# Performance work log

Hardware: AMD Instinct MI355X
Metric: run time of the kernel (lower is better)

Reference implementation:

```python
import jax, jax.numpy as jnp
import numpy as np

N_STATE = 256   # complex state size n (real state is 2n)
N_IN = 128
BATCH = 16
T_STEPS = 2048
H_STEP = 0.01
EPS = 1e-3
LAM_RE_MIN, LAM_RE_MAX, MAX_PHASE = -5.0, -0.5, 6.283


def setup_inputs() -> dict:
    rng = np.random.default_rng(0)
    n, nu = N_STATE, N_IN
    # trainable params (as in torch __init__)
    u1 = rng.random(n)
    u2 = rng.random(n) * 2.0 - 1.0
    alpha = np.log(-(u1 * (LAM_RE_MAX - LAM_RE_MIN) + LAM_RE_MIN)).astype(np.float32)
    theta = (MAX_PHASE * u2).astype(np.float32)
    B_re = (rng.standard_normal((n, nu)) / np.sqrt(2.0 * nu)).astype(np.float32)
    B_im = (rng.standard_normal((n, nu)) / np.sqrt(2.0 * nu)).astype(np.float32)
    # fixed basis-change buffers: rho (normalized), T_inv, P = rho @ T_inv, Pinv
    H1 = rng.standard_normal((n, n))
    H2 = rng.standard_normal((n, n))
    rho = np.block([[H1, -H2], [H2, H1]])
    rho = rho / np.linalg.norm(rho)
    I = np.eye(n)
    T_inv = (1.0 / np.sqrt(2.0)) * np.block([[I, I], [-1j * I, 1j * I]])
    P = rho.astype(np.complex128) @ T_inv
    Pinv = np.linalg.inv(P)
    key = jax.random.key(0)
    k1, k2 = jax.random.split(key)
    return {
        "xi_init": jax.random.normal(k1, (BATCH, 1, 2 * n), dtype=jnp.float32),
        "u_log": jax.random.normal(k2, (BATCH, T_STEPS, nu), dtype=jnp.float32),
        "alpha": jnp.asarray(alpha),
        "theta": jnp.asarray(theta),
        "B_re": jnp.asarray(B_re),
        "B_im": jnp.asarray(B_im),
        "P_re": jnp.asarray(P.real, dtype=jnp.float32),
        "P_im": jnp.asarray(P.imag, dtype=jnp.float32),
        "Pinv_re": jnp.asarray(Pinv.real, dtype=jnp.float32),
        "Pinv_im": jnp.asarray(Pinv.imag, dtype=jnp.float32),
        "T": T_STEPS,
    }


def reference(xi_init, u_log, alpha, theta, B_re, B_im, P_re, P_im, Pinv_re, Pinv_im, T):
    n = alpha.shape[0]
    lam = (-jnp.exp(alpha) - EPS) + 1j * theta          # (n,) complex64
    Bc = B_re + 1j * B_im                               # (n, nu)
    P = P_re + 1j * P_im                                # (2n, 2n)
    Pinv = Pinv_re + 1j * Pinv_im                       # (2n, 2n)
    xi0 = xi_init[:, 0, :]                              # (B, 2n) real

    def step(xi, u_t):
        # xi: (B, 2n) real state; u_t: (B, nu)
        x_tilde = xi.astype(jnp.complex64) @ Pinv.T     # (B, 2n) complex
        x_bar = x_tilde[:, :n]                          # (B, n)
        x_bar_dot = lam * x_bar + u_t.astype(jnp.complex64) @ Bc.T
        x_tilde_dot = jnp.concatenate([x_bar_dot, jnp.conj(x_bar_dot)], axis=-1)
        x_dot = (x_tilde_dot @ P.T).real                # (B, 2n)
        xi_new = xi + H_STEP * x_dot
        return xi_new, xi_new

    u_seq = jnp.swapaxes(u_log, 0, 1)                   # (T, B, nu)
    _, xs = jax.lax.scan(step, xi0, u_seq)              # (T, B, 2n)
    # torch _sim logs xi_init, then skips xi after t=0, logs xi after t=1..T-1
    x_log = jnp.concatenate([xi0[None], xs[1:]], axis=0)  # (T, B, 2n)
    return jnp.swapaxes(x_log, 0, 1)                    # (B, T, 2n)
```

## Files before the change

### kernel.cpp

```cpp
#include <hip/hip_runtime.h>
#include <hip/hip_bf16.h>
#include <cstddef>
#include <cstdint>

#define N_ST 256
#define TWO_N 512
#define NU 128
#define BATCH 16
#define TSTEPS 2048
#define MTOT (BATCH * TSTEPS)
#define H_STEP 0.01f
#define EPS_V 0.001f
#define NCHUNK 32
#define CHUNKL 64

typedef __attribute__((ext_vector_type(4))) float f32x4;
typedef __attribute__((ext_vector_type(4))) short s16x4;
typedef __attribute__((ext_vector_type(8))) short s16x8;

#define AS1 __attribute__((address_space(1)))
#define AS3 __attribute__((address_space(3)))

#define OFF_FPK    0
#define OFF_ZPK    8388608
#define OFF_UPK    16777216
#define OFF_WT     18874368
#define OFF_WF     19005440
#define OFF_D      19038208
#define OFF_XBAR0  19039232
#define OFF_E      19047424

static __device__ __forceinline__ float bf2f(short s) {
    return __uint_as_float(((unsigned)(unsigned short)s) << 16);
}
static __device__ __forceinline__ short f2bf(float f) {
    __hip_bfloat16 b = __float2bfloat16(f);
    return *reinterpret_cast<short*>(&b);
}

__global__ __launch_bounds__(256) void prep_mega(
    const float* __restrict__ P_re, const float* __restrict__ P_im,
    const float* __restrict__ B_re, const float* __restrict__ B_im,
    const float* __restrict__ alpha, const float* __restrict__ theta,
    const float* __restrict__ Pinv_re, const float* __restrict__ Pinv_im,
    const float* __restrict__ xi0, const float* __restrict__ u,
    short* __restrict__ Wtpk, short* __restrict__ Wfpk,
    float* __restrict__ dbuf, float* __restrict__ xbar0,
    short* __restrict__ upk)
{
    __shared__ float xs[BATCH * TWO_N];
    int blk = blockIdx.x, tid = threadIdx.x;
    if (blk < 1024) {
        int idx = blk * 256 + tid;
        int j = idx >> 9, c = idx & 511;
        float v;
        if (c < N_ST) v = P_re[j * TWO_N + c] + P_re[j * TWO_N + c + N_ST];
        else          v = P_im[j * TWO_N + c] - P_im[j * TWO_N + c - N_ST];
        Wtpk[((size_t)(j >> 4) * TWO_N + c) * 16 + (j & 15)] = f2bf(v);
    } else if (blk < 1280) {
        int idx = (blk - 1024) * 256 + tid;
        int k = idx >> 9, c = idx & 511;
        float v = (c < N_ST) ? B_re[c * NU + k] : B_im[(c - N_ST) * NU + k];
        Wfpk[((size_t)(c >> 4) * NU + k) * 16 + (c & 15)] = f2bf(H_STEP * v);
    } else if (blk == 1280) {
        int i = tid;
        float dr = 1.0f + H_STEP * (-expf(alpha[i]) - EPS_V);
        float di = H_STEP * theta[i];
        float pr = 1.0f, pi = 0.0f;
        for (int k = 0; k < CHUNKL; ++k) { float nr = pr * dr - pi * di; pi = pr * di + pi * dr; pr = nr; }
        dbuf[i] = dr; dbuf[N_ST + i] = di; dbuf[2 * N_ST + i] = pr; dbuf[3 * N_ST + i] = pi;
    } else if (blk < 1345) {
#pragma unroll
        for (int q = 0; q < 8; ++q)
            *reinterpret_cast<float4*>(&xs[(q * 256 + tid) * 4]) =
                *reinterpret_cast<const float4*>(&xi0[(q * 256 + tid) * 4]);
        __syncthreads();
        int wv = tid >> 6, l = tid & 63;
        int i = (blk - 1281) * 4 + wv;
        float rp[BATCH] = {}, ip[BATCH] = {};
#pragma unroll
        for (int q = 0; q < 8; ++q) {
            int j = q * 64 + l;
            float pr = Pinv_re[(size_t)i * TWO_N + j];
            float pi = Pinv_im[(size_t)i * TWO_N + j];
#pragma unroll
            for (int b = 0; b < BATCH; ++b) {
                float x = xs[b * TWO_N + j];
                rp[b] = fmaf(pr, x, rp[b]);
                ip[b] = fmaf(pi, x, ip[b]);
            }
        }
#pragma unroll
        for (int m = 1; m < 64; m <<= 1) {
#pragma unroll
            for (int b = 0; b < BATCH; ++b) {
                rp[b] += __shfl_xor(rp[b], m, 64);
                ip[b] += __shfl_xor(ip[b], m, 64);
            }
        }
        if (l == 0) {
#pragma unroll
            for (int b = 0; b < BATCH; ++b) {
                xbar0[b * TWO_N + i] = rp[b];
                xbar0[b * TWO_N + N_ST + i] = ip[b];
            }
        }
    } else {
        short* st = (short*)xs;
        int bid = blk - 1345;
        const float* up = u + (size_t)bid * 8192;
#pragma unroll
        for (int q = 0; q < 8; ++q) {
            int idx = q * 1024 + tid * 4;
            float4 v = *reinterpret_cast<const float4*>(up + idx);
            int m = idx >> 7, k = idx & 127;
            s16x4 pv;
            pv[0] = f2bf(v.x); pv[1] = f2bf(v.y); pv[2] = f2bf(v.z); pv[3] = f2bf(v.w);
            *reinterpret_cast<__shared__ s16x4*>(&st[m * 132 + k]) = pv;
        }
        __syncthreads();
        short* op = upk + (size_t)bid * 8192;
#pragma unroll
        for (int q2 = 0; q2 < 4; ++q2) {
            int o = q2 * 2048 + tid * 8;
            int ml = o & 15, k = (o >> 4) & 127, sl = o >> 11;
            s16x8 w;
#pragma unroll
            for (int r = 0; r < 8; ++r) w[r] = st[(sl * 16 + ml + r) * 132 + k];
            *reinterpret_cast<s16x8*>(op + o) = w;
        }
    }
}

__global__ __launch_bounds__(512, 2) void chunk_fgemm(
    const short* __restrict__ upk, const short* __restrict__ Wfpk,
    const float* __restrict__ dbuf, short* __restrict__ Fpk,
    float* __restrict__ e)
{
    __shared__ __align__(1024) short lds[36864];
    char* smem = (char*)lds;
    const int tid = threadIdx.x;
    const int w = tid >> 6, lane = tid & 63;
    const int laneL = lane & 15, laneH = lane >> 4;
    const int cid = blockIdx.x;
    const unsigned ldsA = (unsigned)(uintptr_t)(AS3 short*)&lds[0];
    f32x4 acc[4][4] = {};

#define STG(buf, kk)                                                                                \
    do {                                                                                            \
        _Pragma("unroll")                                                                           \
        for (int q_ = 0; q_ < 4; ++q_) {                                                            \
            int sb_ = w + q_ * 8;                                                                   \
            __builtin_amdgcn_global_load_lds(                                                       \
                (const AS1 void*)(Wfpk + (size_t)sb_ * 2048 + (size_t)(kk) * 16 + lane * 8),        \
                (AS3 void*)(smem + 8192 + (buf) * 32768 + sb_ * 1024), 16, 0, 0);                   \
        }                                                                                           \
        if (w < 4) {                                                                                \
            __builtin_amdgcn_global_load_lds(                                                       \
                (const AS1 void*)(upk + (size_t)(cid * 4 + w) * 2048 + (size_t)(kk) * 16 + lane * 8), \
                (AS3 void*)(smem + (buf) * 4096 + w * 1024), 16, 0, 0);                             \
        }                                                                                           \
    } while (0)

    STG(0, 0);
#pragma unroll
    for (int t = 0; t < 4; ++t) {
        const int buf = t & 1;
        if (t < 3) STG(buf ^ 1, (t + 1) * 32);
        if (t < 3) {
            if (w < 4) asm volatile("s_waitcnt vmcnt(5)" ::: "memory");
            else       asm volatile("s_waitcnt vmcnt(4)" ::: "memory");
        } else {
            asm volatile("s_waitcnt vmcnt(0)" ::: "memory");
        }
        __builtin_amdgcn_sched_barrier(0);
        __builtin_amdgcn_s_barrier();
        __builtin_amdgcn_sched_barrier(0);

        s16x4 al[4], ah[4], bl[4], bh[4];
#pragma unroll
        for (int i = 0; i < 4; ++i) {
            unsigned ad = ldsA + (unsigned)buf * 4096u + (unsigned)i * 1024u + ((unsigned)lane << 3);
            asm volatile("ds_read_b64_tr_b16 %0, %1 offset:0"   : "=v"(al[i]) : "v"(ad));
            asm volatile("ds_read_b64_tr_b16 %0, %1 offset:512" : "=v"(ah[i]) : "v"(ad));
        }
#pragma unroll
        for (int j = 0; j < 4; ++j) {
            unsigned bd = ldsA + 8192u + (unsigned)buf * 32768u + ((unsigned)(w * 4 + j) << 10) + ((unsigned)lane << 3);
            asm volatile("ds_read_b64_tr_b16 %0, %1 offset:0"   : "=v"(bl[j]) : "v"(bd));
            asm volatile("ds_read_b64_tr_b16 %0, %1 offset:512" : "=v"(bh[j]) : "v"(bd));
        }
        asm volatile("s_waitcnt lgkmcnt(0)" ::: "memory");
        __builtin_amdgcn_sched_barrier(0);
        __builtin_amdgcn_s_barrier();
        __builtin_amdgcn_sched_barrier(0);

        __builtin_amdgcn_s_setprio(1);
#pragma unroll
        for (int i = 0; i < 4; ++i) {
            s16x8 av = __builtin_shufflevector(al[i], ah[i], 0, 1, 2, 3, 4, 5, 6, 7);
#pragma unroll
            for (int j = 0; j < 4; ++j) {
                s16x8 bv = __builtin_shufflevector(bl[j], bh[j], 0, 1, 2, 3, 4, 5, 6, 7);
                acc[i][j] = __builtin_amdgcn_mfma_f32_16x16x32_bf16(av, bv, acc[i][j], 0, 0, 0);
            }
        }
        __builtin_amdgcn_s_setprio(0);
    }
#undef STG

    const int g4 = laneH * 4;
#pragma unroll
    for (int i = 0; i < 4; ++i) {
        size_t slab = (size_t)(cid * 4 + i);
#pragma unroll
        for (int j = 0; j < 4; ++j) {
            int n = w * 64 + j * 16 + laneL;
            s16x4 pv;
#pragma unroll
            for (int r = 0; r < 4; ++r) pv[r] = f2bf(acc[i][j][r]);
            *reinterpret_cast<s16x4*>(Fpk + slab * 8192 + (size_t)n * 16 + g4) = pv;
        }
    }
#pragma unroll
    for (int i = 0; i < 4; ++i) {
#pragma unroll
        for (int j = 0; j < 4; ++j) {
            int s = w * 64 + j * 16 + laneL;
#pragma unroll
            for (int r = 0; r < 4; ++r) {
                int t = i * 16 + laneH * 4 + r;
                *(short*)(smem + t * 1024 + (((unsigned)(2 * s)) ^ (unsigned)((t & 15) << 3))) =
                    f2bf(acc[i][j][r]);
            }
        }
    }
    __syncthreads();
    if (tid < 256) {
        const int i2 = tid;
        float dr = dbuf[i2], di = dbuf[N_ST + i2];
        float re = 0.f, im = 0.f;
        const unsigned colr = (unsigned)(2 * i2);
#pragma unroll 8
        for (int t = 0; t < CHUNKL; ++t) {
            char* p = smem + t * 1024 + (colr ^ (unsigned)((t & 15) << 3));
            float fr = bf2f(*(short*)p);
            float fi = bf2f(*(short*)(p + 512));
            float nre = fmaf(dr, re, fmaf(-di, im, fr));
            float nim = fmaf(dr, im, fmaf(di, re, fi));
            re = nre; im = nim;
        }
        e[(size_t)cid * TWO_N + i2] = re;
        e[(size_t)cid * TWO_N + N_ST + i2] = im;
    }
}

__global__ __launch_bounds__(256) void scan_passC(const short* __restrict__ Fpk,
                                                  const float* __restrict__ dbuf,
                                                  const float* __restrict__ e,
                                                  const float* __restrict__ xbar0,
                                                  short* __restrict__ Zpk) {
    int b = blockIdx.x, c = blockIdx.y, i = threadIdx.x;
    float dr = dbuf[i], di = dbuf[N_ST + i];
    float dLr = dbuf[2 * N_ST + i], dLi = dbuf[3 * N_ST + i];
    float re = xbar0[b * TWO_N + i], im = xbar0[b * TWO_N + N_ST + i];
    for (int cc = 0; cc < c; ++cc) {
        size_t o = ((size_t)(b * NCHUNK + cc)) * TWO_N;
        float er = e[o + i], ei = e[o + N_ST + i];
        float nre = fmaf(dLr, re, fmaf(-dLi, im, er));
        float nim = fmaf(dLr, im, fmaf(dLi, re, ei));
        re = nre; im = nim;
    }
    int slab0 = (b * TSTEPS + c * CHUNKL) >> 4;
#pragma unroll
    for (int g = 0; g < 4; ++g) {
        const short* base = Fpk + (size_t)(slab0 + g) * 8192 + i * 16;
        s16x8 r0 = *reinterpret_cast<const s16x8*>(base);
        s16x8 r1 = *reinterpret_cast<const s16x8*>(base + 8);
        s16x8 i0 = *reinterpret_cast<const s16x8*>(base + 4096);
        s16x8 i1 = *reinterpret_cast<const s16x8*>(base + 4096 + 8);
        s16x8 zr0, zr1, zi0, zi1;
#pragma unroll
        for (int j = 0; j < 16; ++j) {
            float fr = bf2f(j < 8 ? r0[j & 7] : r1[j & 7]);
            float fi = bf2f(j < 8 ? i0[j & 7] : i1[j & 7]);
            float nre = fmaf(dr, re, fmaf(-di, im, fr));
            float nim = fmaf(dr, im, fmaf(di, re, fi));
            re = nre; im = nim;
            if (j < 8) { zr0[j & 7] = f2bf(re); zi0[j & 7] = f2bf(im); }
            else       { zr1[j & 7] = f2bf(re); zi1[j & 7] = f2bf(im); }
        }
        short* zb = Zpk + (size_t)(slab0 + g) * 8192 + i * 16;
        *reinterpret_cast<s16x8*>(zb)            = zr0;
        *reinterpret_cast<s16x8*>(zb + 8)        = zr1;
        *reinterpret_cast<s16x8*>(zb + 4096)     = zi0;
        *reinterpret_cast<s16x8*>(zb + 4096 + 8) = zi1;
    }
}

__global__ __launch_bounds__(512, 2) void gemm_out(const short* __restrict__ Apk,
                                                   const short* __restrict__ Bpk,
                                                   float* __restrict__ Cf,
                                                   const float* __restrict__ xi0) {
    __shared__ __align__(1024) short lds[49152];
    const int tid = threadIdx.x;
    const int wid = tid >> 6, lane = tid & 63;
    const int l = blockIdx.x;
    const int mb = ((l >> 4) << 3) | (l & 7);
    const int nb = (l >> 3) & 1;
    const int m0 = mb * 256, n0 = nb * 256;
    const int wm = wid >> 2, wn = wid & 3;
    f32x4 acc[8][4] = {};
    const size_t slabStride = (size_t)TWO_N * 16;
    const unsigned ldsBase = (unsigned)(uintptr_t)(AS3 short*)&lds[0];
    constexpr int NT = TWO_N / 32;

#define STAGE(buf, kk)                                                                              \
    do {                                                                                            \
        const short* gA0 = Apk + ((size_t)(m0 >> 4) + wid)     * slabStride + (size_t)(kk) * 16 + lane * 8; \
        const short* gA1 = Apk + ((size_t)(m0 >> 4) + wid + 8) * slabStride + (size_t)(kk) * 16 + lane * 8; \
        const short* gB0 = Bpk + ((size_t)(n0 >> 4) + wid)     * slabStride + (size_t)(kk) * 16 + lane * 8; \
        const short* gB1 = Bpk + ((size_t)(n0 >> 4) + wid + 8) * slabStride + (size_t)(kk) * 16 + lane * 8; \
        __builtin_amdgcn_global_load_lds((const AS1 void*)gA0,                                      \
            (AS3 void*)&lds[(buf) * 8192 + wid * 512], 16, 0, 0);                                   \
        __builtin_amdgcn_global_load_lds((const AS1 void*)gA1,                                      \
            (AS3 void*)&lds[(buf) * 8192 + (wid + 8) * 512], 16, 0, 0);                             \
        __builtin_amdgcn_global_load_lds((const AS1 void*)gB0,                                      \
            (AS3 void*)&lds[24576 + (buf) * 8192 + wid * 512], 16, 0, 0);                           \
        __builtin_amdgcn_global_load_lds((const AS1 void*)gB1,                                      \
            (AS3 void*)&lds[24576 + (buf) * 8192 + (wid + 8) * 512], 16, 0, 0);                     \
    } while (0)

    STAGE(0, 0);
    STAGE(1, 32);

#pragma unroll
    for (int t = 0; t < NT; ++t) {
        const int cur = t % 3;
        if (t + 2 < NT) STAGE((t + 2) % 3, (t + 2) * 32);

        if (t + 2 < NT)      asm volatile("s_waitcnt vmcnt(8)" ::: "memory");
        else if (t + 1 < NT) asm volatile("s_waitcnt vmcnt(4)" ::: "memory");
        else                 asm volatile("s_waitcnt vmcnt(0)" ::: "memory");
        __builtin_amdgcn_sched_barrier(0);
        __builtin_amdgcn_s_barrier();
        __builtin_amdgcn_sched_barrier(0);

        s16x4 al[8], ah[8], bl[4], bh[4];
        const unsigned aB = ldsBase + (unsigned)cur * 16384u;
        const unsigned bB = ldsBase + 49152u + (unsigned)cur * 16384u;
#pragma unroll
        for (int i = 0; i < 8; ++i) {
            unsigned ad = aB + ((unsigned)(wm * 8 + i) << 10) + ((unsigned)lane << 3);
            asm volatile("ds_read_b64_tr_b16 %0, %1 offset:0"   : "=v"(al[i]) : "v"(ad));
            asm volatile("ds_read_b64_tr_b16 %0, %1 offset:512" : "=v"(ah[i]) : "v"(ad));
        }
#pragma unroll
        for (int j = 0; j < 4; ++j) {
            unsigned bd = bB + ((unsigned)(wn * 4 + j) << 10) + ((unsigned)lane << 3);
            asm volatile("ds_read_b64_tr_b16 %0, %1 offset:0"   : "=v"(bl[j]) : "v"(bd));
            asm volatile("ds_read_b64_tr_b16 %0, %1 offset:512" : "=v"(bh[j]) : "v"(bd));
        }
        asm volatile("s_waitcnt lgkmcnt(0)" ::: "memory");
        __builtin_amdgcn_sched_barrier(0);
        __builtin_amdgcn_s_barrier();
        __builtin_amdgcn_sched_barrier(0);

        __builtin_amdgcn_s_setprio(1);
#pragma unroll
        for (int i = 0; i < 8; ++i) {
            s16x8 av = __builtin_shufflevector(al[i], ah[i], 0, 1, 2, 3, 4, 5, 6, 7);
#pragma unroll
            for (int j = 0; j < 4; ++j) {
                s16x8 bv = __builtin_shufflevector(bl[j], bh[j], 0, 1, 2, 3, 4, 5, 6, 7);
                acc[i][j] = __builtin_amdgcn_mfma_f32_16x16x32_bf16(av, bv, acc[i][j], 0, 0, 0);
            }
        }
        __builtin_amdgcn_s_setprio(0);
    }
#undef STAGE

    const int cn = lane & 15;
    const int g4 = (lane >> 4) * 4;
#pragma unroll
    for (int i = 0; i < 8; ++i) {
        int mrow = m0 + wm * 128 + i * 16 + g4;
#pragma unroll
        for (int j = 0; j < 4; ++j) {
            int ncol = n0 + wn * 64 + j * 16 + cn;
            float* cp = Cf + (size_t)mrow * TWO_N + ncol;
#pragma unroll
            for (int r = 0; r < 4; ++r) {
                float v = acc[i][j][r];
                if (((mrow + r) & (TSTEPS - 1)) == 0)
                    v = xi0[((mrow + r) >> 11) * TWO_N + ncol];
                cp[(size_t)r * TWO_N] = v;
            }
        }
    }
}

extern "C" void kernel_launch(void* const* d_in, const int* in_sizes, int n_in,
                              void* d_out, int out_size, void* d_ws, size_t ws_size,
                              hipStream_t stream) {
    const float* xi_init = (const float*)d_in[0];
    const float* u_log   = (const float*)d_in[1];
    const float* alpha   = (const float*)d_in[2];
    const float* theta   = (const float*)d_in[3];
    const float* B_re    = (const float*)d_in[4];
    const float* B_im    = (const float*)d_in[5];
    const float* P_re    = (const float*)d_in[6];
    const float* P_im    = (const float*)d_in[7];
    const float* Pinv_re = (const float*)d_in[8];
    const float* Pinv_im = (const float*)d_in[9];
    float* out = (float*)d_out;
    float* ws  = (float*)d_ws;

    short* Fpk  = (short*)(ws + OFF_FPK);
    short* Zpk  = (short*)(ws + OFF_ZPK);
    short* upk  = (short*)(ws + OFF_UPK);
    short* Wtpk = (short*)(ws + OFF_WT);
    short* Wfpk = (short*)(ws + OFF_WF);
    float* dbuf  = ws + OFF_D;
    float* xbar0 = ws + OFF_XBAR0;
    float* e     = ws + OFF_E;

    prep_mega<<<1857, 256, 0, stream>>>(P_re, P_im, B_re, B_im, alpha, theta,
                                        Pinv_re, Pinv_im, xi_init, u_log,
                                        Wtpk, Wfpk, dbuf, xbar0, upk);

    chunk_fgemm<<<MTOT / CHUNKL, 512, 0, stream>>>(upk, Wfpk, dbuf, Fpk, e);

    scan_passC<<<dim3(BATCH, NCHUNK), 256, 0, stream>>>(Fpk, dbuf, e, xbar0, Zpk);

    gemm_out<<<256, 512, 0, stream>>>(Zpk, Wtpk, out, xi_init);
}
```

Baseline: 71.78 us.

## Recompute chunk GEMM in second pass and fuse scan, dropping F buffer

Replaces the separate F-buffer write and scan_passC kernel with a templated chunk kernel launched twice. The first pass computes chunk end-states e. The second recomputes the chunk GEMM, carries the prefix across chunks, and scans directly from LDS to emit Z. This removes the round trip of the large bf16 F intermediate through global memory. In exchange the input GEMM and the u loads are done twice.

```diff
diff --git a/kernel.cpp b/kernel.cpp
--- a/kernel.cpp
+++ b/kernel.cpp
@@ -21,14 +21,13 @@
 #define AS1 __attribute__((address_space(1)))
 #define AS3 __attribute__((address_space(3)))
 
-#define OFF_FPK    0
-#define OFF_ZPK    8388608
-#define OFF_UPK    16777216
-#define OFF_WT     18874368
-#define OFF_WF     19005440
-#define OFF_D      19038208
-#define OFF_XBAR0  19039232
-#define OFF_E      19047424
+#define OFF_ZPK    0
+#define OFF_UPK    8388608
+#define OFF_WT     10485760
+#define OFF_WF     10616832
+#define OFF_D      10649600
+#define OFF_XBAR0  10650624
+#define OFF_E      10658816
 
 static __device__ __forceinline__ float bf2f(short s) {
     return __uint_as_float(((unsigned)(unsigned short)s) << 16);
@@ -132,10 +131,11 @@
     }
 }
 
-__global__ __launch_bounds__(512, 2) void chunk_fgemm(
+template <bool EMITZ>
+__global__ __launch_bounds__(512, 2) void chunk_fs(
     const short* __restrict__ upk, const short* __restrict__ Wfpk,
-    const float* __restrict__ dbuf, short* __restrict__ Fpk,
-    float* __restrict__ e)
+    const float* __restrict__ dbuf, float* __restrict__ e,
+    const float* __restrict__ xbar0, short* __restrict__ Zpk)
 {
     __shared__ __align__(1024) short lds[36864];
     char* smem = (char*)lds;
@@ -209,19 +209,6 @@
     }
 #undef STG
 
-    const int g4 = laneH * 4;
-#pragma unroll
-    for (int i = 0; i < 4; ++i) {
-        size_t slab = (size_t)(cid * 4 + i);
-#pragma unroll
-        for (int j = 0; j < 4; ++j) {
-            int n = w * 64 + j * 16 + laneL;
-            s16x4 pv;
-#pragma unroll
-            for (int r = 0; r < 4; ++r) pv[r] = f2bf(acc[i][j][r]);
-            *reinterpret_cast<s16x4*>(Fpk + slab * 8192 + (size_t)n * 16 + g4) = pv;
-        }
-    }
 #pragma unroll
     for (int i = 0; i < 4; ++i) {
 #pragma unroll
@@ -236,65 +223,63 @@
         }
     }
     __syncthreads();
-    if (tid < 256) {
-        const int i2 = tid;
-        float dr = dbuf[i2], di = dbuf[N_ST + i2];
-        float re = 0.f, im = 0.f;
-        const unsigned colr = (unsigned)(2 * i2);
+
+    if (!EMITZ) {
+        if (tid < 256) {
+            const int i2 = tid;
+            float dr = dbuf[i2], di = dbuf[N_ST + i2];
+            float re = 0.f, im = 0.f;
+            const unsigned colr = (unsigned)(2 * i2);
 #pragma unroll 8
-        for (int t = 0; t < CHUNKL; ++t) {
-            char* p = smem + t * 1024 + (colr ^ (unsigned)((t & 15) << 3));
-            float fr = bf2f(*(short*)p);
-            float fi = bf2f(*(short*)(p + 512));
-            float nre = fmaf(dr, re, fmaf(-di, im, fr));
-            float nim = fmaf(dr, im, fmaf(di, re, fi));
-            re = nre; im = nim;
-        }
-        e[(size_t)cid * TWO_N + i2] = re;
-        e[(size_t)cid * TWO_N + N_ST + i2] = im;
-    }
-}
-
-__global__ __launch_bounds__(256) void scan_passC(const short* __restrict__ Fpk,
-                                                  const float* __restrict__ dbuf,
-                                                  const float* __restrict__ e,
-                                                  const float* __restrict__ xbar0,
-                                                  short* __restrict__ Zpk) {
-    int b = blockIdx.x, c = blockIdx.y, i = threadIdx.x;
-    float dr = dbuf[i], di = dbuf[N_ST + i];
-    float dLr = dbuf[2 * N_ST + i], dLi = dbuf[3 * N_ST + i];
-    float re = xbar0[b * TWO_N + i], im = xbar0[b * TWO_N + N_ST + i];
-    for (int cc = 0; cc < c; ++cc) {
-        size_t o = ((size_t)(b * NCHUNK + cc)) * TWO_N;
-        float er = e[o + i], ei = e[o + N_ST + i];
-        float nre = fmaf(dLr, re, fmaf(-dLi, im, er));
-        float nim = fmaf(dLr, im, fmaf(dLi, re, ei));
-        re = nre; im = nim;
-    }
-    int slab0 = (b * TSTEPS + c * CHUNKL) >> 4;
-#pragma unroll
-    for (int g = 0; g < 4; ++g) {
-        const short* base = Fpk + (size_t)(slab0 + g) * 8192 + i * 16;
-        s16x8 r0 = *reinterpret_cast<const s16x8*>(base);
-        s16x8 r1 = *reinterpret_cast<const s16x8*>(base + 8);
-        s16x8 i0 = *reinterpret_cast<const s16x8*>(base + 4096);
-        s16x8 i1 = *reinterpret_cast<const s16x8*>(base + 4096 + 8);
-        s16x8 zr0, zr1, zi0, zi1;
-#pragma unroll
-        for (int j = 0; j < 16; ++j) {
-            float fr = bf2f(j < 8 ? r0[j & 7] : r1[j & 7]);
-            float fi = bf2f(j < 8 ? i0[j & 7] : i1[j & 7]);
-            float nre = fmaf(dr, re, fmaf(-di, im, fr));
-            float nim = fmaf(dr, im, fmaf(di, re, fi));
-            re = nre; im = nim;
-            if (j < 8) { zr0[j & 7] = f2bf(re); zi0[j & 7] = f2bf(im); }
-            else       { zr1[j & 7] = f2bf(re); zi1[j & 7] = f2bf(im); }
-        }
-        short* zb = Zpk + (size_t)(slab0 + g) * 8192 + i * 16;
-        *reinterpret_cast<s16x8*>(zb)            = zr0;
-        *reinterpret_cast<s16x8*>(zb + 8)        = zr1;
-        *reinterpret_cast<s16x8*>(zb + 4096)     = zi0;
-        *reinterpret_cast<s16x8*>(zb + 4096 + 8) = zi1;
+            for (int t = 0; t < CHUNKL; ++t) {
+                char* p = smem + t * 1024 + (colr ^ (unsigned)((t & 15) << 3));
+                float fr = bf2f(*(short*)p);
+                float fi = bf2f(*(short*)(p + 512));
+                float nre = fmaf(dr, re, fmaf(-di, im, fr));
+                float nim = fmaf(dr, im, fmaf(di, re, fi));
+                re = nre; im = nim;
+            }
+            e[(size_t)cid * TWO_N + i2] = re;
+            e[(size_t)cid * TWO_N + N_ST + i2] = im;
+        }
+    } else {
+        if (tid < 256) {
+            const int i2 = tid;
+            const int b = cid >> 5, c = cid & 31;
+            float dr = dbuf[i2], di = dbuf[N_ST + i2];
+            float dLr = dbuf[2 * N_ST + i2], dLi = dbuf[3 * N_ST + i2];
+            float re = xbar0[b * TWO_N + i2], im = xbar0[b * TWO_N + N_ST + i2];
+            for (int cc = 0; cc < c; ++cc) {
+                size_t o = ((size_t)(b * NCHUNK + cc)) * TWO_N;
+                float er = e[o + i2], ei = e[o + N_ST + i2];
+                float nre = fmaf(dLr, re, fmaf(-dLi, im, er));
+                float nim = fmaf(dLr, im, fmaf(dLi, re, ei));
+                re = nre; im = nim;
+            }
+            const unsigned colr = (unsigned)(2 * i2);
+            int slab0 = cid * 4;
+#pragma unroll
+            for (int g = 0; g < 4; ++g) {
+                s16x8 zr0, zr1, zi0, zi1;
+#pragma unroll
+                for (int jj = 0; jj < 16; ++jj) {
+                    int t = g * 16 + jj;
+                    char* p = smem + t * 1024 + (colr ^ (unsigned)((t & 15) << 3));
+                    float fr = bf2f(*(short*)p);
+                    float fi = bf2f(*(short*)(p + 512));
+                    float nre = fmaf(dr, re, fmaf(-di, im, fr));
+                    float nim = fmaf(dr, im, fmaf(di, re, fi));
+                    re = nre; im = nim;
+                    if (jj < 8) { zr0[jj & 7] = f2bf(re); zi0[jj & 7] = f2bf(im); }
+                    else        { zr1[jj & 7] = f2bf(re); zi1[jj & 7] = f2bf(im); }
+                }
+                short* zb = Zpk + (size_t)(slab0 + g) * 8192 + i2 * 16;
+                *reinterpret_cast<s16x8*>(zb)            = zr0;
+                *reinterpret_cast<s16x8*>(zb + 8)        = zr1;
+                *reinterpret_cast<s16x8*>(zb + 4096)     = zi0;
+                *reinterpret_cast<s16x8*>(zb + 4096 + 8) = zi1;
+            }
+        }
     }
 }
 
@@ -416,7 +401,6 @@
     float* out = (float*)d_out;
     float* ws  = (float*)d_ws;
 
-    short* Fpk  = (short*)(ws + OFF_FPK);
     short* Zpk  = (short*)(ws + OFF_ZPK);
     short* upk  = (short*)(ws + OFF_UPK);
     short* Wtpk = (short*)(ws + OFF_WT);
@@ -429,9 +413,9 @@
                                         Pinv_re, Pinv_im, xi_init, u_log,
                                         Wtpk, Wfpk, dbuf, xbar0, upk);
 
-    chunk_fgemm<<<MTOT / CHUNKL, 512, 0, stream>>>(upk, Wfpk, dbuf, Fpk, e);
-
-    scan_passC<<<dim3(BATCH, NCHUNK), 256, 0, stream>>>(Fpk, dbuf, e, xbar0, Zpk);
+    chunk_fs<false><<<MTOT / CHUNKL, 512, 0, stream>>>(upk, Wfpk, dbuf, e, xbar0, Zpk);
+
+    chunk_fs<true><<<MTOT / CHUNKL, 512, 0, stream>>>(upk, Wfpk, dbuf, e, xbar0, Zpk);
 
     gemm_out<<<256, 512, 0, stream>>>(Zpk, Wtpk, out, xi_init);
 }
```

New measurement: 77.47 us. +7.9%, slower.
